# Kernel tuning notes

Measured on AMD Instinct MI355X. Metric: run time of the kernel, lower is better.

Reference implementation:

```python
import jax, jax.numpy as jnp
import numpy as np

H = W = 256          # full-res feature map (2h x 2w)
WIN = 16             # window size
STRIDE = 2           # shifted-window stride
HEADS = 8
DIM_HEAD = 64
INNER = HEADS * DIM_HEAD
DIM = 128
KEEP = 50            # min(int(0.7*(256//16)**2), 50)
IOU_THR = 0.2


def _make_windows():
    xs = np.arange(0, W - WIN + 1, STRIDE)
    ys = np.arange(0, H - WIN + 1, STRIDE)
    gx, gy = np.meshgrid(xs, ys)
    return np.stack([gx.ravel(), gy.ravel(), gx.ravel() + WIN - 1, gy.ravel() + WIN - 1], axis=1)

_WIN_NP = _make_windows()          # [M,4] = (x1,y1,x2,y2), M = 121*121 = 14641
BOXES = jnp.asarray(_WIN_NP, dtype=jnp.float32)
SXY = jnp.asarray(_WIN_NP[:, :2], dtype=jnp.int32)   # integer (sx, sy) origins

# torchvision roi_align (spatial_scale=1, sampling_ratio->ceil(15/16)=1, aligned=False):
_off = (np.arange(WIN) + 0.5) * (WIN - 1.0) / WIN
LO = jnp.asarray(np.floor(_off).astype(np.int32))      # low integer index, in [0,14]
FR = jnp.asarray((_off - np.floor(_off)).astype(np.float32))


def _nms_keep(scores):
    """Greedy NMS over the fixed window grid; returns top-KEEP kept indices."""
    x1, y1, x2, y2 = BOXES[:, 0], BOXES[:, 1], BOXES[:, 2], BOXES[:, 3]
    area = (x2 - x1) * (y2 - y1)

    def body(k, carry):
        live, keep = carry
        idx = jnp.argmax(jnp.where(live, scores, -jnp.inf))
        bb = BOXES[idx]
        iw = jnp.clip(jnp.minimum(x2, bb[2]) - jnp.maximum(x1, bb[0]), 0.0)
        ih = jnp.clip(jnp.minimum(y2, bb[3]) - jnp.maximum(y1, bb[1]), 0.0)
        inter = iw * ih
        iou = inter / (area + area[idx] - inter)
        live = live & (iou <= IOU_THR)
        return live, keep.at[k].set(idx.astype(jnp.int32))

    _, keep = jax.lax.fori_loop(
        0, KEEP, body,
        (jnp.ones(BOXES.shape[0], bool), jnp.zeros(KEEP, jnp.int32)))
    return keep


def _forward(x, prob, fix_w, w_qkv, w_out, b_out):
    b = prob.shape[0]
    d = x.shape[-1]
    # entropy map at half res
    entropy = -jnp.sum(prob * jnp.log2(prob + 1e-10), axis=1)          # [b,128,128]
    # FixCNN: 8x8 ones-init conv, VALID -> [b,1,121,121]; normalized window score
    score = jax.lax.conv_general_dilated(
        entropy[:, None], fix_w, (1, 1), 'VALID',
        dimension_numbers=('NCHW', 'OIHW', 'NCHW'))
    score = score.reshape(b, -1) / float((WIN // 2) * (WIN // 2))      # [b,14641]

    keep = jax.lax.stop_gradient(jax.vmap(_nms_keep)(score))           # [b,KEEP]
    sx = SXY[keep][..., 0]                                             # [b,KEEP]
    sy = SXY[keep][..., 1]

    x2d = x.reshape(b, H, W, d)   # token n = h*W + w (channels-last layout)
    ar = jnp.arange(WIN)

    def gather_one(xi, syi, sxi):  # xi [H,W,d]
        R = syi[:, None, None] + ar[None, :, None]
        C = sxi[:, None, None] + ar[None, None, :]
        return xi[R, C]

    crops = jax.vmap(gather_one)(x2d, sy, sx)                          # [b,K,16,16,d]

    # roi_align bilinear sampling with fixed fractional grid
    c00 = crops[:, :, LO[:, None], LO[None, :]]
    c01 = crops[:, :, LO[:, None], LO[None, :] + 1]
    c10 = crops[:, :, LO[:, None] + 1, LO[None, :]]
    c11 = crops[:, :, LO[:, None] + 1, LO[None, :] + 1]
    fy = FR[:, None, None]
    fx = FR[None, :, None]
    win = ((1 - fy) * (1 - fx) * c00 + (1 - fy) * fx * c01
           + fy * (1 - fx) * c10 + fy * fx * c11)                      # [b,K,16,16,d]

    toks = win.reshape(b * KEEP, WIN * WIN, d)                         # [m,256,d]
    qkv = toks @ w_qkv.T                                               # [m,256,3*INNER]
    q, k_, v = jnp.split(qkv, 3, axis=-1)

    def to_heads(t):
        return t.reshape(t.shape[0], t.shape[1], HEADS, DIM_HEAD).transpose(0, 2, 1, 3)

    q, k_, v = to_heads(q), to_heads(k_), to_heads(v)
    attn = jax.nn.softmax(jnp.einsum('mhnd,mhkd->mhnk', q, k_) * (DIM_HEAD ** -0.5), axis=-1)
    out = jnp.einsum('mhnk,mhkd->mhnd', attn, v)
    out = out.transpose(0, 2, 1, 3).reshape(b * KEEP, WIN * WIN, INNER)
    out = out @ w_out.T + b_out                                        # [m,256,d]

    # overlap scatter-add + count normalization
    out2d = out.reshape(b, KEEP, WIN, WIN, d)
    bidx = jnp.arange(b)[:, None, None, None]
    Y = sy[:, :, None, None] + ar[None, None, :, None]
    X = sx[:, :, None, None] + ar[None, None, None, :]
    acc = jnp.zeros((b, H, W, d), x.dtype).at[bidx, Y, X].add(out2d)
    cnt = jnp.zeros((b, H, W), x.dtype).at[bidx, Y, X].add(1.0)
    outx = (acc / (cnt[..., None] + 1e-10)).reshape(b, H * W, d)
    return x + outx


def setup_inputs() -> dict:
    key = jax.random.key(0)
    ks = jax.random.split(key, 4)
    b = 4
    x = jax.random.normal(ks[0], (b, H * W, DIM), dtype=jnp.float32)
    prob = jax.random.uniform(ks[1], (b, 2, H // 2, W // 2), dtype=jnp.float32)
    fix_w = jnp.ones((1, 1, WIN // 2, WIN // 2), dtype=jnp.float32)
    w_qkv = jax.random.normal(ks[2], (3 * INNER, DIM), dtype=jnp.float32) * 0.02
    w_out = jax.random.normal(ks[3], (DIM, INNER), dtype=jnp.float32) * 0.02
    b_out = jnp.zeros((DIM,), dtype=jnp.float32)
    return {"x": x, "prob": prob, "fix_w": fix_w, "w_qkv": w_qkv, "w_out": w_out, "b_out": b_out}


def reference(x, prob, fix_w, w_qkv, w_out, b_out):
    return _forward(x, prob, fix_w, w_qkv, w_out, b_out)
```

## Files before the change

### kernel.cpp

```cpp
#include <hip/hip_runtime.h>
#include <math.h>

#define NB 4
#define NWIN 121
#define NBOX (NWIN*NWIN)
#define NKEEP 50
#define HWD 256
#define DIM 128
#define HEADS 8
#define NTOK 256
#define NWTOT (NB*NKEEP)
#define SCPAD 15616

#define OFF_ENT   0
#define OFF_SCORE 65536
#define OFF_KEEP  128128
#define OFF_WQKV  128256
#define OFF_WOUT  226560
#define OFF_TOKBF 259328
#define OFF_PO    3536128
#define WS_FLOATS 6812928

#define KPAD 76
#define VPAD 268
#define KP3 68
#define VP3 132

typedef __attribute__((ext_vector_type(8))) short short8;
typedef __attribute__((ext_vector_type(4))) short short4v;
typedef __attribute__((ext_vector_type(4))) float f32x4;

static __device__ __forceinline__ unsigned short f2bf(float f) {
  union { float f; unsigned u; } v; v.f = f;
  unsigned r = (v.u + 0x7fffu + ((v.u >> 16) & 1u)) >> 16;
  return (unsigned short)r;
}
static __device__ __forceinline__ short4v pk4(f32x4 a) {
  short4v r;
  r[0] = (short)f2bf(a[0]); r[1] = (short)f2bf(a[1]);
  r[2] = (short)f2bf(a[2]); r[3] = (short)f2bf(a[3]);
  return r;
}
static __device__ __forceinline__ short8 ld8_lds(const unsigned short* p) {
  short4v a = *(const short4v*)p;
  short4v b = *(const short4v*)(p + 4);
  short8 r;
  r[0]=a[0]; r[1]=a[1]; r[2]=a[2]; r[3]=a[3];
  r[4]=b[0]; r[5]=b[1]; r[6]=b[2]; r[7]=b[3];
  return r;
}
static __device__ __forceinline__ short8 ld8_g(const unsigned short* p) {
  return *(const short8*)p;
}

template<int CTRL>
static __device__ __forceinline__ float dppmax(float v) {
  union { float f; int i; } a, r; a.f = v;
  r.i = __builtin_amdgcn_update_dpp(a.i, a.i, CTRL, 0xf, 0xf, false);
  return fmaxf(v, r.f);
}
static __device__ __forceinline__ float wavemax(float v) {
  v = dppmax<0x111>(v); v = dppmax<0x112>(v);
  v = dppmax<0x114>(v); v = dppmax<0x118>(v);
  v = dppmax<0x142>(v); v = dppmax<0x143>(v);
  union { float f; int i; } gi, gm; gi.f = v;
  gm.i = __builtin_amdgcn_readlane(gi.i, 63);
  return gm.f;
}

__global__ void k_entropy(const float* __restrict__ prob, float* __restrict__ ent) {
  int idx = blockIdx.x * 256 + threadIdx.x;
  int b = idx >> 14, p = idx & 16383;
  float p0 = prob[(size_t)(b * 2) * 16384 + p];
  float p1 = prob[(size_t)(b * 2 + 1) * 16384 + p];
  ent[idx] = -(p0 * log2f(p0 + 1e-10f) + p1 * log2f(p1 + 1e-10f));
}

__global__ void k_score(const float* __restrict__ ent, const float* __restrict__ fw,
                        float* __restrict__ scp) {
  int gid = blockIdx.x * 256 + threadIdx.x;
  if (gid >= NB * SCPAD) return;
  int b = gid / SCPAD, idx = gid % SCPAD;
  int r = idx >> 7, c = idx & 127;
  float s = -INFINITY;
  if (r < NWIN && c < NWIN) {
    const float* e = ent + b * 16384 + r * 128 + c;
    float a = 0.f;
#pragma unroll
    for (int rr = 0; rr < 8; ++rr)
#pragma unroll
      for (int cc = 0; cc < 8; ++cc)
        a += e[rr * 128 + cc] * fw[rr * 8 + cc];
    s = a * (1.0f / 64.0f);
  }
  scp[b * SCPAD + (r << 7) + (c ^ ((r & 7) << 2))] = s;
}

__global__ void k_nms(const float* __restrict__ scp, int* __restrict__ keep) {
  __shared__ float sc[SCPAD];
  int b = blockIdx.x, l = threadIdx.x;
  const float* src = scp + b * SCPAD;
  for (int cb = 0; cb < 64; cb += 8) {
    f32x4 t[8];
#pragma unroll
    for (int i = 0; i < 8; ++i) {
      int idx = (cb + i) * 256 + l * 4;
      if (idx < SCPAD) t[i] = *(const f32x4*)&src[idx];
    }
#pragma unroll
    for (int i = 0; i < 8; ++i) {
      int idx = (cb + i) * 256 + l * 4;
      if (idx < SCPAD) *(f32x4*)&sc[idx] = t[i];
    }
  }
  float M0 = -INFINITY, M1 = -INFINITY; int C0 = 0, C1 = 0;
#pragma unroll
  for (int slot = 0; slot < 2; ++slot) {
    int r = l + slot * 64;
    if (slot == 1 && r >= NWIN) break;
    int r7 = (r & 7) << 2, rbase = r << 7;
    float bv0=-INFINITY,bv1=-INFINITY,bv2=-INFINITY,bv3=-INFINITY;
    int bc0=0,bc1=0,bc2=0,bc3=0;
    for (int lb = 0; lb < 32; ++lb) {
      f32x4 v = *(const f32x4*)&sc[rbase + ((lb << 2) ^ r7)];
      int c0 = lb << 2;
      if (v[0] > bv0) { bv0 = v[0]; bc0 = c0; }
      if (v[1] > bv1) { bv1 = v[1]; bc1 = c0 + 1; }
      if (v[2] > bv2) { bv2 = v[2]; bc2 = c0 + 2; }
      if (v[3] > bv3) { bv3 = v[3]; bc3 = c0 + 3; }
    }
    float bv = bv0; int bc = bc0;
    if (bv1 > bv || (bv1 == bv && bc1 < bc)) { bv = bv1; bc = bc1; }
    if (bv2 > bv || (bv2 == bv && bc2 < bc)) { bv = bv2; bc = bc2; }
    if (bv3 > bv || (bv3 == bv && bc3 < bc)) { bv = bv3; bc = bc3; }
    if (slot == 0) { M0 = bv; C0 = bc; } else { M1 = bv; C1 = bc; }
  }
  for (int k = 0; k < NKEEP; ++k) {
    float gmax = wavemax(fmaxf(M0, M1));
    unsigned long long b0 = __ballot(M0 == gmax);
    unsigned long long b1 = __ballot(M1 == gmax);
    int R;
    if (b0) R = __ffsll((unsigned long long)b0) - 1;
    else    R = 64 + __ffsll((unsigned long long)b1) - 1;
    int Cc = (R < 64) ? __builtin_amdgcn_readlane(C0, R)
                      : __builtin_amdgcn_readlane(C1, R - 64);
    if (l == 0) {
      keep[(b * NKEEP + k) * 2 + 0] = 2 * R;
      keep[(b * NKEEP + k) * 2 + 1] = 2 * Cc;
    }
    bool kill0 = false, kill1 = false;
    {
      int dy = l - R, ady = dy < 0 ? -dy : dy;
      if (ady <= 4) {
        int ih = 15 - 2 * ady;
#pragma unroll
        for (int dx = -4; dx <= 4; ++dx) {
          int adx = dx < 0 ? -dx : dx;
          if ((15 - 2 * adx) * ih > 75) {
            int cc = Cc + dx;
            if ((unsigned)cc < (unsigned)NWIN)
              sc[(l << 7) + (cc ^ ((l & 7) << 2))] = -INFINITY;
          }
        }
        int adx = C0 - Cc; adx = adx < 0 ? -adx : adx;
        kill0 = (adx <= 4) && ((15 - 2 * adx) * ih > 75);
      }
    }
    if (l + 64 < NWIN) {
      int r1 = l + 64;
      int dy = r1 - R, ady = dy < 0 ? -dy : dy;
      if (ady <= 4) {
        int ih = 15 - 2 * ady;
#pragma unroll
        for (int dx = -4; dx <= 4; ++dx) {
          int adx = dx < 0 ? -dx : dx;
          if ((15 - 2 * adx) * ih > 75) {
            int cc = Cc + dx;
            if ((unsigned)cc < (unsigned)NWIN)
              sc[(r1 << 7) + (cc ^ ((r1 & 7) << 2))] = -INFINITY;
          }
        }
        int adx = C1 - Cc; adx = adx < 0 ? -adx : adx;
        kill1 = (adx <= 4) && ((15 - 2 * adx) * ih > 75);
      }
    }
    unsigned long long need0 = __ballot(kill0);
    unsigned long long need1 = __ballot(kill1);
    while (need0 | need1) {
      int rr;
      if (need0) { rr = __ffsll((unsigned long long)need0) - 1; need0 &= need0 - 1; }
      else       { rr = __ffsll((unsigned long long)need1) - 1 + 64; need1 &= need1 - 1; }
      int r7 = (rr & 7) << 2, rbase = rr << 7;
      float v0 = sc[rbase + (l ^ r7)];
      float v1 = sc[rbase + ((l + 64) ^ r7)];
      float rmax = wavemax(fmaxf(v0, v1));
      unsigned long long e0 = __ballot(v0 == rmax);
      unsigned long long e1 = __ballot(v1 == rmax);
      int bc;
      if (e0) bc = __ffsll((unsigned long long)e0) - 1;
      else    bc = 64 + __ffsll((unsigned long long)e1) - 1;
      if (l == (rr & 63)) {
        if (rr >= 64) { M1 = rmax; C1 = bc; }
        else          { M0 = rmax; C0 = bc; }
      }
    }
  }
}

__global__ void k_wcvt(const float* __restrict__ wqkv, const float* __restrict__ wout,
                       unsigned short* __restrict__ wqkv_bf, unsigned short* __restrict__ wout_bf) {
  int i = blockIdx.x * 256 + threadIdx.x;
  if (i < 196608) wqkv_bf[i] = f2bf(wqkv[i]);
  int j = i - 196608;
  if (j >= 0 && j < 65536) wout_bf[j] = f2bf(wout[j]);
}

__global__ void k_toks(const float* __restrict__ x, const int* __restrict__ keep,
                       unsigned short* __restrict__ tokbf) {
  int w = blockIdx.x;
  int b = w / NKEEP;
  int sy = keep[w * 2 + 0], sx = keep[w * 2 + 1];
  int tid = threadIdx.x;
  int ch = tid & 127, th = tid >> 7;
  const float* xb = x + (size_t)b * 65536 * DIM;
  for (int it = 0; it < 128; ++it) {
    int tk = it * 2 + th;
    int i = tk >> 4, j = tk & 15;
    float offy = (i + 0.5f) * 0.9375f;
    float offx = (j + 0.5f) * 0.9375f;
    int li = (int)offy, lj = (int)offx;
    float fy = offy - (float)li, fx = offx - (float)lj;
    const float* p = xb + ((size_t)((sy + li) * HWD + (sx + lj))) * DIM + ch;
    float v00 = p[0], v01 = p[DIM], v10 = p[HWD * DIM], v11 = p[HWD * DIM + DIM];
    float w00 = (1.f - fy) * (1.f - fx), w01 = (1.f - fy) * fx;
    float w10 = fy * (1.f - fx), w11 = fy * fx;
    tokbf[((size_t)w * NTOK + tk) * DIM + ch] = f2bf(w00 * v00 + w01 * v01 + w10 * v10 + w11 * v11);
  }
}

__global__ __launch_bounds__(512, 2) void k_attn3(
    const unsigned short* __restrict__ tokbf,
    const unsigned short* __restrict__ wqkv,
    const unsigned short* __restrict__ wout,
    unsigned short* __restrict__ po) {
  __shared__ __align__(16) char smem[51712];
  unsigned short* Kh  = (unsigned short*)smem;
  unsigned short* VTh = (unsigned short*)(smem + 17408);
  const int tid = threadIdx.x;
  const int wv = tid >> 6, ln = tid & 63, lo = ln & 15, hi = ln >> 4;
  const int bid = blockIdx.x;
  const int win = bid >> 1, qh = bid & 1;
  unsigned short* QP = (unsigned short*)(smem + 34304 + wv * 2176);
  const unsigned short* tw = tokbf + (size_t)win * NTOK * DIM;
  const int qb = qh * 128 + wv * 16;

  f32x4 pacc[8];
#pragma unroll
  for (int mf = 0; mf < 8; ++mf) pacc[mf] = (f32x4){0.f,0.f,0.f,0.f};

  for (int h = 0; h < HEADS; ++h) {
    {
      f32x4 qacc[4];
#pragma unroll
      for (int mf = 0; mf < 4; ++mf) qacc[mf] = (f32x4){0.f,0.f,0.f,0.f};
#pragma unroll
      for (int kf = 0; kf < 4; ++kf) {
        short8 bt = ld8_g(&tw[(qb + lo) * 128 + kf * 32 + hi * 8]);
#pragma unroll
        for (int mf = 0; mf < 4; ++mf) {
          short8 aw = ld8_g(wqkv + (size_t)(h * 64 + mf * 16 + lo) * 128 + kf * 32 + hi * 8);
          qacc[mf] = __builtin_amdgcn_mfma_f32_16x16x32_bf16(aw, bt, qacc[mf], 0, 0, 0);
        }
      }
#pragma unroll
      for (int mf = 0; mf < 4; ++mf)
        *(short4v*)&QP[lo * KP3 + mf * 16 + hi * 4] = pk4(qacc[mf] * 0.125f);
    }
    short8 Qb[2];
#pragma unroll
    for (int kf = 0; kf < 2; ++kf)
      Qb[kf] = ld8_lds(&QP[lo * KP3 + kf * 32 + hi * 8]);

    f32x4 Ot[4];
#pragma unroll
    for (int mf = 0; mf < 4; ++mf) Ot[mf] = (f32x4){0.f,0.f,0.f,0.f};
    float mrow = -INFINITY, lrow = 0.f;

    for (int half = 0; half < 2; ++half) {
      __syncthreads();
      const int kbase = half * 128 + wv * 16;
      {
        f32x4 kacc[4];
#pragma unroll
        for (int mf = 0; mf < 4; ++mf) kacc[mf] = (f32x4){0.f,0.f,0.f,0.f};
#pragma unroll
        for (int kf = 0; kf < 4; ++kf) {
          short8 bt = ld8_g(&tw[(kbase + lo) * 128 + kf * 32 + hi * 8]);
#pragma unroll
          for (int mf = 0; mf < 4; ++mf) {
            short8 aw = ld8_g(wqkv + (size_t)(512 + h * 64 + mf * 16 + lo) * 128 + kf * 32 + hi * 8);
            kacc[mf] = __builtin_amdgcn_mfma_f32_16x16x32_bf16(aw, bt, kacc[mf], 0, 0, 0);
          }
        }
#pragma unroll
        for (int mf = 0; mf < 4; ++mf)
          *(short4v*)&Kh[(wv * 16 + lo) * KP3 + mf * 16 + hi * 4] = pk4(kacc[mf]);
      }
      {
        f32x4 vacc[4];
#pragma unroll
        for (int nf = 0; nf < 4; ++nf) vacc[nf] = (f32x4){0.f,0.f,0.f,0.f};
#pragma unroll
        for (int kf = 0; kf < 4; ++kf) {
          short8 at = ld8_g(&tw[(kbase + lo) * 128 + kf * 32 + hi * 8]);
#pragma unroll
          for (int nf = 0; nf < 4; ++nf) {
            short8 bw = ld8_g(wqkv + (size_t)(1024 + h * 64 + nf * 16 + lo) * 128 + kf * 32 + hi * 8);
            vacc[nf] = __builtin_amdgcn_mfma_f32_16x16x32_bf16(at, bw, vacc[nf], 0, 0, 0);
          }
        }
#pragma unroll
        for (int nf = 0; nf < 4; ++nf)
          *(short4v*)&VTh[(nf * 16 + lo) * VP3 + wv * 16 + hi * 4] = pk4(vacc[nf]);
      }
      __syncthreads();

      for (int ck = 0; ck < 2; ++ck) {
        f32x4 sacc[4];
#pragma unroll
        for (int mf = 0; mf < 4; ++mf) sacc[mf] = (f32x4){0.f,0.f,0.f,0.f};
#pragma unroll
        for (int kf = 0; kf < 2; ++kf) {
          short8 ka[4];
#pragma unroll
          for (int mf = 0; mf < 4; ++mf)
            ka[mf] = ld8_lds(&Kh[(ck * 64 + mf * 16 + lo) * KP3 + kf * 32 + hi * 8]);
#pragma unroll
          for (int mf = 0; mf < 4; ++mf)
            sacc[mf] = __builtin_amdgcn_mfma_f32_16x16x32_bf16(ka[mf], Qb[kf], sacc[mf], 0, 0, 0);
        }

        float cmax = -INFINITY;
#pragma unroll
        for (int mf = 0; mf < 4; ++mf)
#pragma unroll
          for (int r = 0; r < 4; ++r) cmax = fmaxf(cmax, sacc[mf][r]);
        cmax = fmaxf(cmax, __shfl_xor(cmax, 16));
        cmax = fmaxf(cmax, __shfl_xor(cmax, 32));
        float mnew = fmaxf(mrow, cmax);
        float corr = __expf(mrow - mnew);
        float ps = 0.f;
#pragma unroll
        for (int mf = 0; mf < 4; ++mf)
#pragma unroll
          for (int r = 0; r < 4; ++r) {
            float e = __expf(sacc[mf][r] - mnew);
            sacc[mf][r] = e; ps += e;
          }
        ps += __shfl_xor(ps, 16);
        ps += __shfl_xor(ps, 32);
        lrow = lrow * corr + ps;
        mrow = mnew;
#pragma unroll
        for (int mf = 0; mf < 4; ++mf) Ot[mf] *= corr;

#pragma unroll
        for (int mf = 0; mf < 4; ++mf)
          *(short4v*)&QP[lo * KP3 + mf * 16 + hi * 4] = pk4(sacc[mf]);
        short8 pb[2];
#pragma unroll
        for (int kf = 0; kf < 2; ++kf)
          pb[kf] = ld8_lds(&QP[lo * KP3 + kf * 32 + hi * 8]);
#pragma unroll
        for (int kf = 0; kf < 2; ++kf) {
          short8 va[4];
#pragma unroll
          for (int mf = 0; mf < 4; ++mf)
            va[mf] = ld8_lds(&VTh[(mf * 16 + lo) * VP3 + ck * 64 + kf * 32 + hi * 8]);
#pragma unroll
          for (int mf = 0; mf < 4; ++mf)
            Ot[mf] = __builtin_amdgcn_mfma_f32_16x16x32_bf16(va[mf], pb[kf], Ot[mf], 0, 0, 0);
        }
      }
    }

    {
      float inv = 1.f / lrow;
#pragma unroll
      for (int mf = 0; mf < 4; ++mf)
        *(short4v*)&QP[lo * KP3 + mf * 16 + hi * 4] = pk4(Ot[mf] * inv);
    }
    short8 Ob[2];
#pragma unroll
    for (int kf = 0; kf < 2; ++kf)
      Ob[kf] = ld8_lds(&QP[lo * KP3 + kf * 32 + hi * 8]);
#pragma unroll
    for (int kf = 0; kf < 2; ++kf) {
#pragma unroll
      for (int mh = 0; mh < 2; ++mh) {
        short8 aw[4];
#pragma unroll
        for (int m4 = 0; m4 < 4; ++m4)
          aw[m4] = ld8_g(wout + (size_t)((mh * 4 + m4) * 16 + lo) * 512 + h * 64 + kf * 32 + hi * 8);
#pragma unroll
        for (int m4 = 0; m4 < 4; ++m4)
          pacc[mh * 4 + m4] = __builtin_amdgcn_mfma_f32_16x16x32_bf16(aw[m4], Ob[kf], pacc[mh * 4 + m4], 0, 0, 0);
      }
    }
  }

#pragma unroll
  for (int mf = 0; mf < 8; ++mf)
    *(short4v*)&po[((size_t)win * NTOK + qb + lo) * 128 + mf * 16 + hi * 4] = pk4(pacc[mf]);
}

__global__ __launch_bounds__(512, 2) void k_attn(
    const unsigned short* __restrict__ tokbf,
    const unsigned short* __restrict__ wqkv,
    const unsigned short* __restrict__ wout,
    unsigned short* __restrict__ po) {
  __shared__ __align__(16) char smem[112128];
  unsigned short* Klds = (unsigned short*)smem;
  unsigned short* VT   = (unsigned short*)(smem + 38912);
  const int tid = threadIdx.x;
  const int wv = tid >> 6, ln = tid & 63;
  const int lo = ln & 15, hi = ln >> 4;
  const int win = blockIdx.x;
  unsigned short* QP = (unsigned short*)(smem + 73216 + wv * 4864);
  const unsigned short* tw = tokbf + (size_t)win * NTOK * DIM;
  const int qrow = wv * 32;

  f32x4 pacc[8][2];
#pragma unroll
  for (int mf = 0; mf < 8; ++mf)
#pragma unroll
    for (int nf = 0; nf < 2; ++nf) pacc[mf][nf] = (f32x4){0.f,0.f,0.f,0.f};

  for (int h = 0; h < HEADS; ++h) {
    if (h) __syncthreads();
    {
      f32x4 kacc[4][2];
#pragma unroll
      for (int mf = 0; mf < 4; ++mf)
#pragma unroll
        for (int nf = 0; nf < 2; ++nf) kacc[mf][nf] = (f32x4){0.f,0.f,0.f,0.f};
#pragma unroll
      for (int kf = 0; kf < 4; ++kf) {
        short8 aw[4], bt[2];
#pragma unroll
        for (int mf = 0; mf < 4; ++mf)
          aw[mf] = ld8_g(wqkv + (size_t)(512 + h * 64 + mf * 16 + lo) * 128 + kf * 32 + hi * 8);
#pragma unroll
        for (int nf = 0; nf < 2; ++nf)
          bt[nf] = ld8_g(&tw[(qrow + nf * 16 + lo) * 128 + kf * 32 + hi * 8]);
#pragma unroll
        for (int mf = 0; mf < 4; ++mf)
#pragma unroll
          for (int nf = 0; nf < 2; ++nf)
            kacc[mf][nf] = __builtin_amdgcn_mfma_f32_16x16x32_bf16(aw[mf], bt[nf], kacc[mf][nf], 0, 0, 0);
      }
#pragma unroll
      for (int mf = 0; mf < 4; ++mf)
#pragma unroll
        for (int nf = 0; nf < 2; ++nf)
          *(short4v*)&Klds[(qrow + nf * 16 + lo) * KPAD + mf * 16 + hi * 4] = pk4(kacc[mf][nf]);
    }
    {
      f32x4 vacc[2][4];
#pragma unroll
      for (int mf = 0; mf < 2; ++mf)
#pragma unroll
        for (int nf = 0; nf < 4; ++nf) vacc[mf][nf] = (f32x4){0.f,0.f,0.f,0.f};
#pragma unroll
      for (int kf = 0; kf < 4; ++kf) {
        short8 at[2], bw[4];
#pragma unroll
        for (int mf = 0; mf < 2; ++mf)
          at[mf] = ld8_g(&tw[(qrow + mf * 16 + lo) * 128 + kf * 32 + hi * 8]);
#pragma unroll
        for (int nf = 0; nf < 4; ++nf)
          bw[nf] = ld8_g(wqkv + (size_t)(1024 + h * 64 + nf * 16 + lo) * 128 + kf * 32 + hi * 8);
#pragma unroll
        for (int mf = 0; mf < 2; ++mf)
#pragma unroll
          for (int nf = 0; nf < 4; ++nf)
            vacc[mf][nf] = __builtin_amdgcn_mfma_f32_16x16x32_bf16(at[mf], bw[nf], vacc[mf][nf], 0, 0, 0);
      }
#pragma unroll
      for (int mf = 0; mf < 2; ++mf)
#pragma unroll
        for (int nf = 0; nf < 4; ++nf)
          *(short4v*)&VT[(nf * 16 + lo) * VPAD + qrow + mf * 16 + hi * 4] = pk4(vacc[mf][nf]);
    }
    {
      f32x4 qacc[4][2];
#pragma unroll
      for (int mf = 0; mf < 4; ++mf)
#pragma unroll
        for (int nf = 0; nf < 2; ++nf) qacc[mf][nf] = (f32x4){0.f,0.f,0.f,0.f};
#pragma unroll
      for (int kf = 0; kf < 4; ++kf) {
        short8 aw[4], bt[2];
#pragma unroll
        for (int mf = 0; mf < 4; ++mf)
          aw[mf] = ld8_g(wqkv + (size_t)(h * 64 + mf * 16 + lo) * 128 + kf * 32 + hi * 8);
#pragma unroll
        for (int nf = 0; nf < 2; ++nf)
          bt[nf] = ld8_g(&tw[(qrow + nf * 16 + lo) * 128 + kf * 32 + hi * 8]);
#pragma unroll
        for (int mf = 0; mf < 4; ++mf)
#pragma unroll
          for (int nf = 0; nf < 2; ++nf)
            qacc[mf][nf] = __builtin_amdgcn_mfma_f32_16x16x32_bf16(aw[mf], bt[nf], qacc[mf][nf], 0, 0, 0);
      }
#pragma unroll
      for (int mf = 0; mf < 4; ++mf)
#pragma unroll
        for (int nf = 0; nf < 2; ++nf)
          *(short4v*)&QP[(nf * 16 + lo) * KPAD + mf * 16 + hi * 4] = pk4(qacc[mf][nf] * 0.125f);
    }
    __syncthreads();

    short8 Qb[2][2];
#pragma unroll
    for (int nf = 0; nf < 2; ++nf)
#pragma unroll
      for (int kf = 0; kf < 2; ++kf)
        Qb[nf][kf] = ld8_lds(&QP[(nf * 16 + lo) * KPAD + kf * 32 + hi * 8]);

    f32x4 Ot[4][2];
#pragma unroll
    for (int mf = 0; mf < 4; ++mf)
#pragma unroll
      for (int nf = 0; nf < 2; ++nf) Ot[mf][nf] = (f32x4){0.f,0.f,0.f,0.f};
    float mrow[2] = {-INFINITY, -INFINITY};
    float lrow[2] = {0.f, 0.f};

    for (int ck = 0; ck < 4; ++ck) {
      f32x4 sacc[4][2];
#pragma unroll
      for (int mf = 0; mf < 4; ++mf)
#pragma unroll
        for (int nf = 0; nf < 2; ++nf) sacc[mf][nf] = (f32x4){0.f,0.f,0.f,0.f};
      short8 ka[4][2];
#pragma unroll
      for (int mf = 0; mf < 4; ++mf)
#pragma unroll
        for (int kf = 0; kf < 2; ++kf)
          ka[mf][kf] = ld8_lds(&Klds[(ck * 64 + mf * 16 + lo) * KPAD + kf * 32 + hi * 8]);
#pragma unroll
      for (int mf = 0; mf < 4; ++mf)
#pragma unroll
        for (int nf = 0; nf < 2; ++nf)
#pragma unroll
          for (int kf = 0; kf < 2; ++kf)
            sacc[mf][nf] = __builtin_amdgcn_mfma_f32_16x16x32_bf16(ka[mf][kf], Qb[nf][kf], sacc[mf][nf], 0, 0, 0);

#pragma unroll
      for (int nf = 0; nf < 2; ++nf) {
        float cmax = -INFINITY;
#pragma unroll
        for (int mf = 0; mf < 4; ++mf)
#pragma unroll
          for (int r = 0; r < 4; ++r) cmax = fmaxf(cmax, sacc[mf][nf][r]);
        cmax = fmaxf(cmax, __shfl_xor(cmax, 16));
        cmax = fmaxf(cmax, __shfl_xor(cmax, 32));
        float mnew = fmaxf(mrow[nf], cmax);
        float corr = __expf(mrow[nf] - mnew);
        float ps = 0.f;
#pragma unroll
        for (int mf = 0; mf < 4; ++mf)
#pragma unroll
          for (int r = 0; r < 4; ++r) {
            float e = __expf(sacc[mf][nf][r] - mnew);
            sacc[mf][nf][r] = e; ps += e;
          }
        ps += __shfl_xor(ps, 16);
        ps += __shfl_xor(ps, 32);
        lrow[nf] = lrow[nf] * corr + ps;
        mrow[nf] = mnew;
#pragma unroll
        for (int mf = 0; mf < 4; ++mf) Ot[mf][nf] *= corr;
      }
#pragma unroll
      for (int mf = 0; mf < 4; ++mf)
#pragma unroll
        for (int nf = 0; nf < 2; ++nf)
          *(short4v*)&QP[(nf * 16 + lo) * KPAD + mf * 16 + hi * 4] = pk4(sacc[mf][nf]);
      short8 pb[2][2], va[4][2];
#pragma unroll
      for (int nf = 0; nf < 2; ++nf)
#pragma unroll
        for (int kf = 0; kf < 2; ++kf)
          pb[nf][kf] = ld8_lds(&QP[(nf * 16 + lo) * KPAD + kf * 32 + hi * 8]);
#pragma unroll
      for (int mf = 0; mf < 4; ++mf)
#pragma unroll
        for (int kf = 0; kf < 2; ++kf)
          va[mf][kf] = ld8_lds(&VT[(mf * 16 + lo) * VPAD + ck * 64 + kf * 32 + hi * 8]);
#pragma unroll
      for (int mf = 0; mf < 4; ++mf)
#pragma unroll
        for (int nf = 0; nf < 2; ++nf)
#pragma unroll
          for (int kf = 0; kf < 2; ++kf)
            Ot[mf][nf] = __builtin_amdgcn_mfma_f32_16x16x32_bf16(va[mf][kf], pb[nf][kf], Ot[mf][nf], 0, 0, 0);
    }

#pragma unroll
    for (int nf = 0; nf < 2; ++nf) {
      float inv = 1.f / lrow[nf];
#pragma unroll
      for (int mf = 0; mf < 4; ++mf)
        *(short4v*)&QP[(nf * 16 + lo) * KPAD + mf * 16 + hi * 4] = pk4(Ot[mf][nf] * inv);
    }
    short8 Ob[2][2];
#pragma unroll
    for (int nf = 0; nf < 2; ++nf)
#pragma unroll
      for (int kf = 0; kf < 2; ++kf)
        Ob[nf][kf] = ld8_lds(&QP[(nf * 16 + lo) * KPAD + kf * 32 + hi * 8]);
#pragma unroll
    for (int kf = 0; kf < 2; ++kf) {
      short8 aw[8];
#pragma unroll
      for (int mf = 0; mf < 8; ++mf)
        aw[mf] = ld8_g(wout + (size_t)(mf * 16 + lo) * 512 + h * 64 + kf * 32 + hi * 8);
#pragma unroll
      for (int mf = 0; mf < 8; ++mf)
#pragma unroll
        for (int nf = 0; nf < 2; ++nf)
          pacc[mf][nf] = __builtin_amdgcn_mfma_f32_16x16x32_bf16(aw[mf], Ob[nf][kf], pacc[mf][nf], 0, 0, 0);
    }
  }
#pragma unroll
  for (int mf = 0; mf < 8; ++mf)
#pragma unroll
    for (int nf = 0; nf < 2; ++nf)
      *(short4v*)&po[((size_t)win * NTOK + qrow + nf * 16 + lo) * 128 + mf * 16 + hi * 4] = pk4(pacc[mf][nf]);
}

__global__ void k_final(const float* __restrict__ x, const unsigned short* __restrict__ po,
                        const int* __restrict__ keep, const float* __restrict__ bout,
                        float* __restrict__ out) {
  __shared__ int kp[2 * NKEEP];
  int tid = threadIdx.x;
  int gid = blockIdx.x * 256 + tid;
  int chq = gid & 3, pix = gid >> 2;
  int b = pix >> 16, pb = pix & 65535, y = pb >> 8, xx = pb & 255;
  if (tid < 2 * NKEEP) kp[tid] = keep[b * 2 * NKEEP + tid];
  __syncthreads();
  float acc[32];
#pragma unroll
  for (int i = 0; i < 32; ++i) acc[i] = 0.f;
  float cnt = 0.f;
  for (int w = 0; w < NKEEP; ++w) {
    int dy = y - kp[2 * w], dx = xx - kp[2 * w + 1];
    if ((unsigned)dy < 16u && (unsigned)dx < 16u) {
      cnt += 1.f;
      const unsigned short* pp = po + ((size_t)(b * NKEEP + w) * NTOK + dy * 16 + dx) * 128 + chq * 32;
#pragma unroll
      for (int k2 = 0; k2 < 4; ++k2) {
        short8 v = ld8_g(pp + k2 * 8);
#pragma unroll
        for (int j = 0; j < 8; ++j) {
          union { unsigned u; float f; } cv;
          cv.u = ((unsigned)(unsigned short)v[j]) << 16;
          acc[k2 * 8 + j] += cv.f;
        }
      }
    }
  }
  size_t base = (size_t)pix * 128 + chq * 32;
  float inv = 1.f / (cnt + 1e-10f);
#pragma unroll
  for (int i = 0; i < 32; ++i)
    out[base + i] = x[base + i] + (acc[i] + cnt * bout[chq * 32 + i]) * inv;
}

extern "C" void kernel_launch(void* const* d_in, const int* in_sizes, int n_in,
                              void* d_out, int out_size, void* d_ws, size_t ws_size,
                              hipStream_t stream) {
  const float* x    = (const float*)d_in[0];
  const float* prob = (const float*)d_in[1];
  const float* fixw = (const float*)d_in[2];
  const float* wqkv = (const float*)d_in[3];
  const float* wout = (const float*)d_in[4];
  const float* bout = (const float*)d_in[5];
  float* out = (float*)d_out;
  float* ws  = (float*)d_ws;
  if (ws_size < (size_t)WS_FLOATS * 4) return;

  float* ent  = ws + OFF_ENT;
  float* scp  = ws + OFF_SCORE;
  int*   keep = (int*)(ws + OFF_KEEP);
  unsigned short* wqkv_bf = (unsigned short*)(ws + OFF_WQKV);
  unsigned short* wout_bf = (unsigned short*)(ws + OFF_WOUT);
  unsigned short* tokbf   = (unsigned short*)(ws + OFF_TOKBF);
  unsigned short* po      = (unsigned short*)(ws + OFF_PO);

  hipFuncAttributes fa;
  int use3 = 0;
  if (hipFuncGetAttributes(&fa, (const void*)k_attn3) == hipSuccess)
    use3 = (fa.numRegs > 0 && fa.numRegs <= 128 && fa.localSizeBytes == 0);

  k_entropy<<<256, 256, 0, stream>>>(prob, ent);
  k_score<<<(NB * SCPAD + 255) / 256, 256, 0, stream>>>(ent, fixw, scp);
  k_wcvt<<<1024, 256, 0, stream>>>(wqkv, wout, wqkv_bf, wout_bf);
  k_nms<<<NB, 64, 0, stream>>>(scp, keep);
  k_toks<<<NWTOT, 256, 0, stream>>>(x, keep, tokbf);
  if (use3)
    k_attn3<<<NWTOT * 2, 512, 0, stream>>>(tokbf, wqkv_bf, wout_bf, po);
  else
    k_attn<<<NWTOT, 512, 0, stream>>>(tokbf, wqkv_bf, wout_bf, po);
  k_final<<<NB * 65536 * 4 / 256, 256, 0, stream>>>(x, po, keep, bout, out);
}
```

Measured before the change: 390.1 us.

## Compute K/V once per window with 1024-thread blocks instead of per query half

The attention kernel now runs one 1024-thread block per window instead of two 512-thread blocks that each covered half the queries. Each block computes the full K and V projections for all 256 tokens once and keeps them in LDS, so the K/V projection is no longer done twice per window. The cost is a larger LDS footprint (about 108KB), one block per CU, and fewer total blocks (200), which may leave CUs underused. Register use must still stay at or under 128 for the new path to be selected.

```diff
diff --git a/kernel.cpp b/kernel.cpp
--- a/kernel.cpp
+++ b/kernel.cpp
@@ -23,8 +23,7 @@
 
 #define KPAD 76
 #define VPAD 268
-#define KP3 68
-#define VP3 132
+#define QP4  68
 
 typedef __attribute__((ext_vector_type(8))) short short8;
 typedef __attribute__((ext_vector_type(4))) short short4v;
@@ -238,27 +237,62 @@
   }
 }
 
-__global__ __launch_bounds__(512, 2) void k_attn3(
+__global__ __launch_bounds__(1024, 1) void k_attn4(
     const unsigned short* __restrict__ tokbf,
     const unsigned short* __restrict__ wqkv,
     const unsigned short* __restrict__ wout,
     unsigned short* __restrict__ po) {
-  __shared__ __align__(16) char smem[51712];
-  unsigned short* Kh  = (unsigned short*)smem;
-  unsigned short* VTh = (unsigned short*)(smem + 17408);
+  __shared__ __align__(16) char smem[108032];
+  unsigned short* Klds = (unsigned short*)smem;
+  unsigned short* VT   = (unsigned short*)(smem + 38912);
   const int tid = threadIdx.x;
   const int wv = tid >> 6, ln = tid & 63, lo = ln & 15, hi = ln >> 4;
-  const int bid = blockIdx.x;
-  const int win = bid >> 1, qh = bid & 1;
-  unsigned short* QP = (unsigned short*)(smem + 34304 + wv * 2176);
+  const int win = blockIdx.x;
+  unsigned short* QP = (unsigned short*)(smem + 73216 + wv * 2176);
   const unsigned short* tw = tokbf + (size_t)win * NTOK * DIM;
-  const int qb = qh * 128 + wv * 16;
+  const int qb = wv * 16;
 
   f32x4 pacc[8];
 #pragma unroll
   for (int mf = 0; mf < 8; ++mf) pacc[mf] = (f32x4){0.f,0.f,0.f,0.f};
 
   for (int h = 0; h < HEADS; ++h) {
+    if (h) __syncthreads();
+
+    {
+      f32x4 kacc[4];
+#pragma unroll
+      for (int mf = 0; mf < 4; ++mf) kacc[mf] = (f32x4){0.f,0.f,0.f,0.f};
+#pragma unroll
+      for (int kf = 0; kf < 4; ++kf) {
+        short8 bt = ld8_g(&tw[(qb + lo) * 128 + kf * 32 + hi * 8]);
+#pragma unroll
+        for (int mf = 0; mf < 4; ++mf) {
+          short8 aw = ld8_g(wqkv + (size_t)(512 + h * 64 + mf * 16 + lo) * 128 + kf * 32 + hi * 8);
+          kacc[mf] = __builtin_amdgcn_mfma_f32_16x16x32_bf16(aw, bt, kacc[mf], 0, 0, 0);
+        }
+      }
+#pragma unroll
+      for (int mf = 0; mf < 4; ++mf)
+        *(short4v*)&Klds[(qb + lo) * KPAD + mf * 16 + hi * 4] = pk4(kacc[mf]);
+    }
+    {
+      f32x4 vacc[4];
+#pragma unroll
+      for (int nf = 0; nf < 4; ++nf) vacc[nf] = (f32x4){0.f,0.f,0.f,0.f};
+#pragma unroll
+      for (int kf = 0; kf < 4; ++kf) {
+        short8 at = ld8_g(&tw[(qb + lo) * 128 + kf * 32 + hi * 8]);
+#pragma unroll
+        for (int nf = 0; nf < 4; ++nf) {
+          short8 bw = ld8_g(wqkv + (size_t)(1024 + h * 64 + nf * 16 + lo) * 128 + kf * 32 + hi * 8);
+          vacc[nf] = __builtin_amdgcn_mfma_f32_16x16x32_bf16(at, bw, vacc[nf], 0, 0, 0);
+        }
+      }
+#pragma unroll
+      for (int nf = 0; nf < 4; ++nf)
+        *(short4v*)&VT[(nf * 16 + lo) * VPAD + qb + hi * 4] = pk4(vacc[nf]);
+    }
     {
       f32x4 qacc[4];
 #pragma unroll
@@ -274,113 +308,75 @@
       }
 #pragma unroll
       for (int mf = 0; mf < 4; ++mf)
-        *(short4v*)&QP[lo * KP3 + mf * 16 + hi * 4] = pk4(qacc[mf] * 0.125f);
+        *(short4v*)&QP[lo * QP4 + mf * 16 + hi * 4] = pk4(qacc[mf] * 0.125f);
     }
     short8 Qb[2];
 #pragma unroll
     for (int kf = 0; kf < 2; ++kf)
-      Qb[kf] = ld8_lds(&QP[lo * KP3 + kf * 32 + hi * 8]);
+      Qb[kf] = ld8_lds(&QP[lo * QP4 + kf * 32 + hi * 8]);
+
+    __syncthreads();
 
     f32x4 Ot[4];
 #pragma unroll
     for (int mf = 0; mf < 4; ++mf) Ot[mf] = (f32x4){0.f,0.f,0.f,0.f};
     float mrow = -INFINITY, lrow = 0.f;
 
-    for (int half = 0; half < 2; ++half) {
-      __syncthreads();
-      const int kbase = half * 128 + wv * 16;
-      {
-        f32x4 kacc[4];
-#pragma unroll
-        for (int mf = 0; mf < 4; ++mf) kacc[mf] = (f32x4){0.f,0.f,0.f,0.f};
-#pragma unroll
-        for (int kf = 0; kf < 4; ++kf) {
-          short8 bt = ld8_g(&tw[(kbase + lo) * 128 + kf * 32 + hi * 8]);
-#pragma unroll
-          for (int mf = 0; mf < 4; ++mf) {
-            short8 aw = ld8_g(wqkv + (size_t)(512 + h * 64 + mf * 16 + lo) * 128 + kf * 32 + hi * 8);
-            kacc[mf] = __builtin_amdgcn_mfma_f32_16x16x32_bf16(aw, bt, kacc[mf], 0, 0, 0);
-          }
+    for (int ck = 0; ck < 4; ++ck) {
+      f32x4 sacc[4];
+#pragma unroll
+      for (int mf = 0; mf < 4; ++mf) sacc[mf] = (f32x4){0.f,0.f,0.f,0.f};
+#pragma unroll
+      for (int kf = 0; kf < 2; ++kf) {
+        short8 ka[4];
+#pragma unroll
+        for (int mf = 0; mf < 4; ++mf)
+          ka[mf] = ld8_lds(&Klds[(ck * 64 + mf * 16 + lo) * KPAD + kf * 32 + hi * 8]);
+#pragma unroll
+        for (int mf = 0; mf < 4; ++mf)
+          sacc[mf] = __builtin_amdgcn_mfma_f32_16x16x32_bf16(ka[mf], Qb[kf], sacc[mf], 0, 0, 0);
+      }
+
+      float cmax = -INFINITY;
+#pragma unroll
+      for (int mf = 0; mf < 4; ++mf)
+#pragma unroll
+        for (int r = 0; r < 4; ++r) cmax = fmaxf(cmax, sacc[mf][r]);
+      cmax = fmaxf(cmax, __shfl_xor(cmax, 16));
+      cmax = fmaxf(cmax, __shfl_xor(cmax, 32));
+      float mnew = fmaxf(mrow, cmax);
+      float corr = __expf(mrow - mnew);
+      float ps = 0.f;
+#pragma unroll
+      for (int mf = 0; mf < 4; ++mf)
+#pragma unroll
+        for (int r = 0; r < 4; ++r) {
+          float e = __expf(sacc[mf][r] - mnew);
+          sacc[mf][r] = e; ps += e;
         }
-#pragma unroll
-        for (int mf = 0; mf < 4; ++mf)
-          *(short4v*)&Kh[(wv * 16 + lo) * KP3 + mf * 16 + hi * 4] = pk4(kacc[mf]);
-      }
-      {
-        f32x4 vacc[4];
-#pragma unroll
-        for (int nf = 0; nf < 4; ++nf) vacc[nf] = (f32x4){0.f,0.f,0.f,0.f};
-#pragma unroll
-        for (int kf = 0; kf < 4; ++kf) {
-          short8 at = ld8_g(&tw[(kbase + lo) * 128 + kf * 32 + hi * 8]);
-#pragma unroll
-          for (int nf = 0; nf < 4; ++nf) {
-            short8 bw = ld8_g(wqkv + (size_t)(1024 + h * 64 + nf * 16 + lo) * 128 + kf * 32 + hi * 8);
-            vacc[nf] = __builtin_amdgcn_mfma_f32_16x16x32_bf16(at, bw, vacc[nf], 0, 0, 0);
-          }
-        }
-#pragma unroll
-        for (int nf = 0; nf < 4; ++nf)
-          *(short4v*)&VTh[(nf * 16 + lo) * VP3 + wv * 16 + hi * 4] = pk4(vacc[nf]);
-      }
-      __syncthreads();
-
-      for (int ck = 0; ck < 2; ++ck) {
-        f32x4 sacc[4];
-#pragma unroll
-        for (int mf = 0; mf < 4; ++mf) sacc[mf] = (f32x4){0.f,0.f,0.f,0.f};
-#pragma unroll
-        for (int kf = 0; kf < 2; ++kf) {
-          short8 ka[4];
-#pragma unroll
-          for (int mf = 0; mf < 4; ++mf)
-            ka[mf] = ld8_lds(&Kh[(ck * 64 + mf * 16 + lo) * KP3 + kf * 32 + hi * 8]);
-#pragma unroll
-          for (int mf = 0; mf < 4; ++mf)
-            sacc[mf] = __builtin_amdgcn_mfma_f32_16x16x32_bf16(ka[mf], Qb[kf], sacc[mf], 0, 0, 0);
-        }
-
-        float cmax = -INFINITY;
-#pragma unroll
-        for (int mf = 0; mf < 4; ++mf)
-#pragma unroll
-          for (int r = 0; r < 4; ++r) cmax = fmaxf(cmax, sacc[mf][r]);
-        cmax = fmaxf(cmax, __shfl_xor(cmax, 16));
-        cmax = fmaxf(cmax, __shfl_xor(cmax, 32));
-        float mnew = fmaxf(mrow, cmax);
-        float corr = __expf(mrow - mnew);
-        float ps = 0.f;
-#pragma unroll
-        for (int mf = 0; mf < 4; ++mf)
-#pragma unroll
-          for (int r = 0; r < 4; ++r) {
-            float e = __expf(sacc[mf][r] - mnew);
-            sacc[mf][r] = e; ps += e;
-          }
-        ps += __shfl_xor(ps, 16);
-        ps += __shfl_xor(ps, 32);
-        lrow = lrow * corr + ps;
-        mrow = mnew;
-#pragma unroll
-        for (int mf = 0; mf < 4; ++mf) Ot[mf] *= corr;
-
-#pragma unroll
-        for (int mf = 0; mf < 4; ++mf)
-          *(short4v*)&QP[lo * KP3 + mf * 16 + hi * 4] = pk4(sacc[mf]);
-        short8 pb[2];
-#pragma unroll
-        for (int kf = 0; kf < 2; ++kf)
-          pb[kf] = ld8_lds(&QP[lo * KP3 + kf * 32 + hi * 8]);
-#pragma unroll
-        for (int kf = 0; kf < 2; ++kf) {
-          short8 va[4];
-#pragma unroll
-          for (int mf = 0; mf < 4; ++mf)
-            va[mf] = ld8_lds(&VTh[(mf * 16 + lo) * VP3 + ck * 64 + kf * 32 + hi * 8]);
-#pragma unroll
-          for (int mf = 0; mf < 4; ++mf)
-            Ot[mf] = __builtin_amdgcn_mfma_f32_16x16x32_bf16(va[mf], pb[kf], Ot[mf], 0, 0, 0);
-        }
+      ps += __shfl_xor(ps, 16);
+      ps += __shfl_xor(ps, 32);
+      lrow = lrow * corr + ps;
+      mrow = mnew;
+#pragma unroll
+      for (int mf = 0; mf < 4; ++mf) Ot[mf] *= corr;
+
+#pragma unroll
+      for (int mf = 0; mf < 4; ++mf)
+        *(short4v*)&QP[lo * QP4 + mf * 16 + hi * 4] = pk4(sacc[mf]);
+      short8 pb[2];
+#pragma unroll
+      for (int kf = 0; kf < 2; ++kf)
+        pb[kf] = ld8_lds(&QP[lo * QP4 + kf * 32 + hi * 8]);
+#pragma unroll
+      for (int kf = 0; kf < 2; ++kf) {
+        short8 va[4];
+#pragma unroll
+        for (int mf = 0; mf < 4; ++mf)
+          va[mf] = ld8_lds(&VT[(mf * 16 + lo) * VPAD + ck * 64 + kf * 32 + hi * 8]);
+#pragma unroll
+        for (int mf = 0; mf < 4; ++mf)
+          Ot[mf] = __builtin_amdgcn_mfma_f32_16x16x32_bf16(va[mf], pb[kf], Ot[mf], 0, 0, 0);
       }
     }
 
@@ -388,12 +384,12 @@
       float inv = 1.f / lrow;
 #pragma unroll
       for (int mf = 0; mf < 4; ++mf)
-        *(short4v*)&QP[lo * KP3 + mf * 16 + hi * 4] = pk4(Ot[mf] * inv);
+        *(short4v*)&QP[lo * QP4 + mf * 16 + hi * 4] = pk4(Ot[mf] * inv);
     }
     short8 Ob[2];
 #pragma unroll
     for (int kf = 0; kf < 2; ++kf)
-      Ob[kf] = ld8_lds(&QP[lo * KP3 + kf * 32 + hi * 8]);
+      Ob[kf] = ld8_lds(&QP[lo * QP4 + kf * 32 + hi * 8]);
 #pragma unroll
     for (int kf = 0; kf < 2; ++kf) {
 #pragma unroll
@@ -700,17 +696,17 @@
   unsigned short* po      = (unsigned short*)(ws + OFF_PO);
 
   hipFuncAttributes fa;
-  int use3 = 0;
-  if (hipFuncGetAttributes(&fa, (const void*)k_attn3) == hipSuccess)
-    use3 = (fa.numRegs > 0 && fa.numRegs <= 128 && fa.localSizeBytes == 0);
+  int use4 = 0;
+  if (hipFuncGetAttributes(&fa, (const void*)k_attn4) == hipSuccess)
+    use4 = (fa.numRegs > 0 && fa.numRegs <= 128 && fa.localSizeBytes == 0);
 
   k_entropy<<<256, 256, 0, stream>>>(prob, ent);
   k_score<<<(NB * SCPAD + 255) / 256, 256, 0, stream>>>(ent, fixw, scp);
   k_wcvt<<<1024, 256, 0, stream>>>(wqkv, wout, wqkv_bf, wout_bf);
   k_nms<<<NB, 64, 0, stream>>>(scp, keep);
   k_toks<<<NWTOT, 256, 0, stream>>>(x, keep, tokbf);
-  if (use3)
-    k_attn3<<<NWTOT * 2, 512, 0, stream>>>(tokbf, wqkv_bf, wout_bf, po);
+  if (use4)
+    k_attn4<<<NWTOT, 1024, 0, stream>>>(tokbf, wqkv_bf, wout_bf, po);
   else
     k_attn<<<NWTOT, 512, 0, stream>>>(tokbf, wqkv_bf, wout_bf, po);
   k_final<<<NB * 65536 * 4 / 256, 256, 0, stream>>>(x, po, keep, bout, out);
```

New measurement: 390.3 us. Within noise of the previous version (+0.1%).
